# Performance work log

Measured on AMD Instinct MI355X. Metric: run time of the kernel, lower is better.

Reference implementation:

```python
import jax, jax.numpy as jnp
import numpy as np

E = 500_000   # total flattened ngram-node occurrences
N = 100_000   # nr_cfg_nodes
D = 256       # cfg_node_encoding_dim


def setup_inputs() -> dict:
    key = jax.random.key(0)
    ks = jax.random.split(key, 6)
    scattered_input = jax.random.normal(ks[0], (E, D), dtype=jnp.float32)
    previous_cfg_nodes_encodings = jax.random.normal(ks[1], (N, D), dtype=jnp.float32)
    W_k = jax.random.normal(ks[2], (D, D), dtype=jnp.float32) / np.float32(np.sqrt(D))
    b_k = jnp.zeros((D,), dtype=jnp.float32)
    W_g = jax.random.normal(ks[3], (2 * D, D), dtype=jnp.float32) / np.float32(np.sqrt(2 * D))
    b_g = jnp.zeros((D,), dtype=jnp.float32)
    indices = jax.random.randint(ks[4], (E,), 0, N, dtype=jnp.int32)
    return {
        "scattered_input": scattered_input,
        "previous_cfg_nodes_encodings": previous_cfg_nodes_encodings,
        "W_k": W_k, "b_k": b_k, "W_g": W_g, "b_g": b_g,
        "indices": indices,
        "nr_cfg_nodes": N,
    }


def reference(scattered_input, previous_cfg_nodes_encodings, W_k, b_k, W_g, b_g, indices, nr_cfg_nodes):
    d = scattered_input.shape[-1]
    # --- ScatterCombiner, method='attn': scatter-softmax attention per CFG node ---
    keys = scattered_input @ W_k + b_k                       # [E, D]
    queries = previous_cfg_nodes_encodings[indices]          # [E, D] gather per occurrence
    scores = jnp.sum(keys * queries, axis=-1) * (1.0 / jnp.sqrt(jnp.float32(d)))  # [E]
    seg_max = jax.ops.segment_max(scores, indices, num_segments=nr_cfg_nodes)     # [N]
    seg_max = jnp.where(jnp.isfinite(seg_max), seg_max, jnp.float32(0.0))         # empty segments
    ex = jnp.exp(scores - seg_max[indices])                  # [E]
    denom = jax.ops.segment_sum(ex, indices, num_segments=nr_cfg_nodes)           # [N]
    probs = ex / jnp.maximum(denom[indices], jnp.float32(1e-9))                   # [E]
    combined = jax.ops.segment_sum(probs[:, None] * scattered_input, indices,
                                   num_segments=nr_cfg_nodes)                     # [N, D]
    # --- StateUpdater: GRU-like sigmoid gate (dropout disabled / eval mode) ---
    gate_in = jnp.concatenate([previous_cfg_nodes_encodings, combined], axis=-1)  # [N, 2D]
    gate = jax.nn.sigmoid(gate_in @ W_g + b_g)               # [N, D]
    return gate * previous_cfg_nodes_encodings + (1.0 - gate) * combined
```

## Files before the change

### kernel.cpp

```cpp
#include <hip/hip_runtime.h>
#include <math.h>

#define D 256
#define LDS_STRIDE 40

typedef __attribute__((ext_vector_type(8))) short short8;
typedef __attribute__((ext_vector_type(4))) float f32x4;

__device__ inline unsigned short f2bf(float f) {
    unsigned int u = __float_as_uint(f);
    u += 0x7fff + ((u >> 16) & 1);
    return (unsigned short)(u >> 16);
}
__device__ inline float bf2f(unsigned short h) {
    return __uint_as_float(((unsigned int)h) << 16);
}

__global__ __launch_bounds__(256)
void k_prep(const float* __restrict__ prev, const float* __restrict__ Wk,
            const float* __restrict__ Wg,
            unsigned short* __restrict__ prev_bf, unsigned short* __restrict__ Wk_bf,
            unsigned short* __restrict__ WgT, int* __restrict__ counts,
            int n8, int nWk8, int Nn, int gPrev, int gWk, int gWgT) {
    int b = blockIdx.x;
    int t = threadIdx.x;
    if (b < gPrev) {
        int i = b * 256 + t;
        if (i < n8) {
            const float4* p = (const float4*)(prev + (size_t)i * 8);
            float4 a = p[0], c = p[1];
            ushort4 o0 = { f2bf(a.x), f2bf(a.y), f2bf(a.z), f2bf(a.w) };
            ushort4 o1 = { f2bf(c.x), f2bf(c.y), f2bf(c.z), f2bf(c.w) };
            ushort4* q = (ushort4*)(prev_bf + (size_t)i * 8);
            q[0] = o0; q[1] = o1;
        }
    } else if (b < gPrev + gWk) {
        int i = (b - gPrev) * 256 + t;
        if (i < nWk8) {
            const float4* p = (const float4*)(Wk + (size_t)i * 8);
            float4 a = p[0], c = p[1];
            ushort4 o0 = { f2bf(a.x), f2bf(a.y), f2bf(a.z), f2bf(a.w) };
            ushort4 o1 = { f2bf(c.x), f2bf(c.y), f2bf(c.z), f2bf(c.w) };
            ushort4* q = (ushort4*)(Wk_bf + (size_t)i * 8);
            q[0] = o0; q[1] = o1;
        }
    } else if (b < gPrev + gWk + gWgT) {
        int r = b - gPrev - gWk;
        int c = t;
        WgT[(size_t)c * (2 * D) + r] = f2bf(Wg[(size_t)r * D + c]);
    } else {
        int i = (b - gPrev - gWk - gWgT) * 256 + t;
        if (i < Nn) counts[i] = 0;
    }
}

template <int K, bool GATE>
__global__ __launch_bounds__(256)
void k_mfma_gemm(const unsigned short* __restrict__ A0,
                 const unsigned short* __restrict__ A1,
                 const unsigned short* __restrict__ Bn,
                 const float* __restrict__ bg,
                 const float* __restrict__ prevf,
                 unsigned short* __restrict__ wq_out,
                 float* __restrict__ outp,
                 int Nrows) {
    __shared__ unsigned short As[64 * LDS_STRIDE];
    __shared__ unsigned short Bs[256 * LDS_STRIDE];

    int tid  = threadIdx.x;
    int wave = tid >> 6;
    int lane = tid & 63;
    int lcol = lane & 15;
    int quad = lane >> 4;
    int row0 = blockIdx.x * 64;

    f32x4 acc[4][4];
    #pragma unroll
    for (int i = 0; i < 4; i++)
        #pragma unroll
        for (int j = 0; j < 4; j++) acc[i][j] = (f32x4){0.f, 0.f, 0.f, 0.f};

    int arow = tid >> 2, ako = (tid & 3) * 8;
    int grow = row0 + arow;

    for (int kk = 0; kk < K; kk += 32) {
        const unsigned short* Asrc = A0;
        int kc = kk;
        if (GATE && kk >= 256) { Asrc = A1; kc = kk - 256; }

        uint4 av = make_uint4(0u, 0u, 0u, 0u);
        if (grow < Nrows) av = *(const uint4*)&Asrc[(size_t)grow * D + kc + ako];
        *(uint4*)&As[arow * LDS_STRIDE + ako] = av;

        #pragma unroll
        for (int i = 0; i < 4; i++) {
            int c = tid + i * 256;
            int brow = c >> 2, bko = (c & 3) * 8;
            *(uint4*)&Bs[brow * LDS_STRIDE + bko] =
                *(const uint4*)&Bn[(size_t)brow * K + kk + bko];
        }
        __syncthreads();

        short8 a[4], b[4];
        #pragma unroll
        for (int mf = 0; mf < 4; mf++)
            a[mf] = *(const short8*)&As[(mf * 16 + lcol) * LDS_STRIDE + quad * 8];
        #pragma unroll
        for (int nf = 0; nf < 4; nf++)
            b[nf] = *(const short8*)&Bs[(wave * 64 + nf * 16 + lcol) * LDS_STRIDE + quad * 8];
        #pragma unroll
        for (int mf = 0; mf < 4; mf++)
            #pragma unroll
            for (int nf = 0; nf < 4; nf++)
                acc[mf][nf] = __builtin_amdgcn_mfma_f32_16x16x32_bf16(
                    a[mf], b[nf], acc[mf][nf], 0, 0, 0);
        __syncthreads();
    }

    if (!GATE) {
        #pragma unroll
        for (int mf = 0; mf < 4; mf++) {
            #pragma unroll
            for (int nf = 0; nf < 4; nf++) {
                int col = wave * 64 + nf * 16 + lcol;
                #pragma unroll
                for (int r = 0; r < 4; r++) {
                    int gr = row0 + mf * 16 + quad * 4 + r;
                    if (gr < Nrows)
                        wq_out[(size_t)gr * D + col] = f2bf(acc[mf][nf][r]);
                }
            }
        }
    } else {
        float bgv[4];
        #pragma unroll
        for (int nf = 0; nf < 4; nf++) bgv[nf] = bg[wave * 64 + nf * 16 + lcol];
        #pragma unroll
        for (int mf = 0; mf < 4; mf++) {
            #pragma unroll
            for (int nf = 0; nf < 4; nf++) {
                int col = wave * 64 + nf * 16 + lcol;
                #pragma unroll
                for (int r = 0; r < 4; r++) {
                    int gr = row0 + mf * 16 + quad * 4 + r;
                    if (gr < Nrows) {
                        size_t o = (size_t)gr * D + col;
                        float logit = acc[mf][nf][r] + bgv[nf];
                        float g = 1.f / (1.f + __expf(-logit));
                        float cb = bf2f(A1[o]);
                        outp[o] = g * prevf[o] + (1.f - g) * cb;
                    }
                }
            }
        }
    }
}

__global__ __launch_bounds__(256)
void k_hist(const int* __restrict__ idx, int* __restrict__ counts,
            int* __restrict__ rank, int E_) {
    int e = blockIdx.x * 256 + threadIdx.x;
    if (e < E_) rank[e] = atomicAdd(&counts[idx[e]], 1);
}

__global__ __launch_bounds__(256)
void k_part(const int* __restrict__ counts, int* __restrict__ chunkSums, int Nn) {
    __shared__ int sd[256];
    int base = blockIdx.x * 1024;
    int t = threadIdx.x;
    int s = 0;
    #pragma unroll
    for (int i = 0; i < 4; i++) {
        int g = base + t + i * 256;
        if (g < Nn) s += counts[g];
    }
    sd[t] = s;
    __syncthreads();
    for (int st = 128; st; st >>= 1) {
        if (t < st) sd[t] += sd[t + st];
        __syncthreads();
    }
    if (t == 0) chunkSums[blockIdx.x] = sd[0];
}

__global__ __launch_bounds__(256)
void k_top(const int* __restrict__ cs, int* __restrict__ co, int P,
           int* __restrict__ offsets, int Nn, int E_) {
    __shared__ int carry;
    __shared__ int ws[4];
    int t = threadIdx.x, lane = t & 63, w = t >> 6;
    if (t == 0) carry = 0;
    __syncthreads();
    for (int base = 0; base < P; base += 256) {
        int i = base + t;
        int v = (i < P) ? cs[i] : 0;
        int orig = v;
        for (int off = 1; off < 64; off <<= 1) {
            int u = __shfl_up(v, off, 64);
            if (lane >= off) v += u;
        }
        if (lane == 63) ws[w] = v;
        __syncthreads();
        int wex = 0;
        for (int k = 0; k < w; k++) wex += ws[k];
        int incl = v + wex;
        if (i < P) co[i] = carry + incl - orig;
        __syncthreads();
        if (t == 255) carry += incl;
        __syncthreads();
    }
    if (t == 0) offsets[Nn] = E_;
}

__global__ __launch_bounds__(256)
void k_off(const int* __restrict__ counts, const int* __restrict__ chunkOff,
           int* __restrict__ offsets, int Nn) {
    int t = threadIdx.x, lane = t & 63, w = t >> 6;
    int base = blockIdx.x * 1024 + t * 4;
    int c[4]; int ts = 0;
    #pragma unroll
    for (int j = 0; j < 4; j++) {
        int g = base + j;
        c[j] = (g < Nn) ? counts[g] : 0;
        ts += c[j];
    }
    int v = ts;
    for (int off = 1; off < 64; off <<= 1) {
        int u = __shfl_up(v, off, 64);
        if (lane >= off) v += u;
    }
    __shared__ int ws[4];
    if (lane == 63) ws[w] = v;
    __syncthreads();
    int wex = 0;
    for (int k = 0; k < w; k++) wex += ws[k];
    int run = chunkOff[blockIdx.x] + wex + v - ts;
    #pragma unroll
    for (int j = 0; j < 4; j++) {
        int g = base + j;
        if (g < Nn) offsets[g] = run;
        run += c[j];
    }
}

__global__ __launch_bounds__(256)
void k_scatter(const int* __restrict__ idx, const int* __restrict__ rank,
               const int* __restrict__ offsets, int* __restrict__ perm, int E_) {
    int e = blockIdx.x * 256 + threadIdx.x;
    if (e < E_) perm[offsets[idx[e]] + rank[e]] = e;
}

__global__ __launch_bounds__(256)
void k_combine(const float* __restrict__ scat, const unsigned short* __restrict__ wq,
               const int* __restrict__ offsets, const int* __restrict__ perm,
               unsigned short* __restrict__ comb, int Nnodes) {
    int wave = threadIdx.x >> 6;
    int lane = threadIdx.x & 63;
    int n = blockIdx.x * 4 + wave;
    if (n >= Nnodes) return;

    ushort4 wu = *(const ushort4*)&wq[(size_t)n * D + lane * 4];
    float4 wqv = { bf2f(wu.x), bf2f(wu.y), bf2f(wu.z), bf2f(wu.w) };
    int beg = offsets[n], end = offsets[n + 1];

    float m = -INFINITY, l = 0.f;
    float4 acc = { 0.f, 0.f, 0.f, 0.f };
    const float scale = 0.0625f;

    if (beg < end) {
        int e0 = perm[beg];
        float4 sv0 = *(const float4*)&scat[(size_t)e0 * D + lane * 4];
        float4 sv1 = sv0;
        if (beg + 1 < end) {
            int e1 = perm[beg + 1];
            sv1 = *(const float4*)&scat[(size_t)e1 * D + lane * 4];
        }
        for (int pos = beg; pos < end; ++pos) {
            float4 cur = sv0;
            sv0 = sv1;
            if (pos + 2 < end) {
                int e2 = perm[pos + 2];
                sv1 = *(const float4*)&scat[(size_t)e2 * D + lane * 4];
            }
            float d = fmaf(cur.x, wqv.x, fmaf(cur.y, wqv.y,
                      fmaf(cur.z, wqv.z, cur.w * wqv.w)));
            #pragma unroll
            for (int off = 32; off; off >>= 1) d += __shfl_xor(d, off, 64);
            float score = d * scale;
            float nm = fmaxf(m, score);
            float al = __expf(m - nm);
            float p  = __expf(score - nm);
            l = fmaf(l, al, p);
            acc.x = fmaf(acc.x, al, p * cur.x);
            acc.y = fmaf(acc.y, al, p * cur.y);
            acc.z = fmaf(acc.z, al, p * cur.z);
            acc.w = fmaf(acc.w, al, p * cur.w);
            m = nm;
        }
    }
    float inv = 1.f / fmaxf(l, 1e-9f);
    ushort4 o = { f2bf(acc.x * inv), f2bf(acc.y * inv),
                  f2bf(acc.z * inv), f2bf(acc.w * inv) };
    *(ushort4*)&comb[(size_t)n * D + lane * 4] = o;
}

extern "C" void kernel_launch(void* const* d_in, const int* in_sizes, int n_in,
                              void* d_out, int out_size, void* d_ws, size_t ws_size,
                              hipStream_t stream) {
    const float* scat = (const float*)d_in[0];
    const float* prev = (const float*)d_in[1];
    const float* Wk   = (const float*)d_in[2];
    const float* Wg   = (const float*)d_in[4];
    const float* bg   = (const float*)d_in[5];
    const int*   idx  = (const int*)d_in[6];

    const int E_ = in_sizes[6];
    const int Nn = in_sizes[1] / D;

    float* out = (float*)d_out;

    char* w = (char*)d_ws;
    auto alloc = [&](size_t bytes) -> char* {
        char* p = w;
        w += (bytes + 255) & ~(size_t)255;
        return p;
    };
    unsigned short* prev_bf = (unsigned short*)alloc((size_t)Nn * D * 2);
    unsigned short* wq_bf   = (unsigned short*)alloc((size_t)Nn * D * 2);
    unsigned short* comb_bf = (unsigned short*)alloc((size_t)Nn * D * 2);
    unsigned short* Wk_bf   = (unsigned short*)alloc((size_t)D * D * 2);
    unsigned short* WgT_bf  = (unsigned short*)alloc((size_t)2 * D * D * 2);
    int*   counts    = (int*)alloc((size_t)Nn * 4);
    int*   offsets   = (int*)alloc(((size_t)Nn + 1) * 4);
    int    P         = (Nn + 1023) / 1024;
    int*   chunkSums = (int*)alloc((size_t)P * 4);
    int*   chunkOff  = (int*)alloc((size_t)P * 4);
    int*   rank      = (int*)alloc((size_t)E_ * 4);
    int*   perm      = (int*)alloc((size_t)E_ * 4);

    int n8    = Nn * D / 8;
    int nWk8  = D * D / 8;
    int gPrev = (n8 + 255) / 256;
    int gWk   = (nWk8 + 255) / 256;
    int gWgT  = 2 * D;
    int gCnt  = (Nn + 255) / 256;
    k_prep<<<gPrev + gWk + gWgT + gCnt, 256, 0, stream>>>(
        prev, Wk, Wg, prev_bf, Wk_bf, WgT_bf, counts,
        n8, nWk8, Nn, gPrev, gWk, gWgT);

    int gb = (E_ + 255) / 256;
    k_hist<<<gb, 256, 0, stream>>>(idx, counts, rank, E_);
    k_part<<<P, 256, 0, stream>>>(counts, chunkSums, Nn);
    k_top<<<1, 256, 0, stream>>>(chunkSums, chunkOff, P, offsets, Nn, E_);
    k_off<<<P, 256, 0, stream>>>(counts, chunkOff, offsets, Nn);
    k_scatter<<<gb, 256, 0, stream>>>(idx, rank, offsets, perm, E_);

    int gm = (Nn + 63) / 64;
    k_mfma_gemm<256, false><<<gm, 256, 0, stream>>>(
        prev_bf, nullptr, Wk_bf, nullptr, nullptr, wq_bf, nullptr, Nn);

    k_combine<<<(Nn + 3) / 4, 256, 0, stream>>>(scat, wq_bf, offsets, perm, comb_bf, Nn);

    k_mfma_gemm<512, true><<<gm, 256, 0, stream>>>(
        prev_bf, comb_bf, WgT_bf, bg, prev, nullptr, out, Nn);
}
```

Baseline: 998.5 us.

## Fuse bf16 conversion into GEMM loads, merge scan kernels, co-launch scatter with GEMM

The separate pass that converted prev to bf16 is removed. The GEMMs now read fp32 prev and convert it while loading tiles into LDS. The three-kernel prefix scan becomes one kernel in which each block re-sums all earlier counts itself. The permutation scatter and the Wk GEMM share one launch as disjoint block ranges, and the combine loop prefetches one row deeper. Together these cut launches and a full N×D round trip, in exchange for redundant prefix reads and twice the A-tile load bytes.

Measured after the change: 1.007 ms. No clear change (+0.8%).

```diff
diff --git a/kernel.cpp b/kernel.cpp
--- a/kernel.cpp
+++ b/kernel.cpp
@@ -17,25 +17,13 @@
 }
 
 __global__ __launch_bounds__(256)
-void k_prep(const float* __restrict__ prev, const float* __restrict__ Wk,
-            const float* __restrict__ Wg,
-            unsigned short* __restrict__ prev_bf, unsigned short* __restrict__ Wk_bf,
-            unsigned short* __restrict__ WgT, int* __restrict__ counts,
-            int n8, int nWk8, int Nn, int gPrev, int gWk, int gWgT) {
+void k_prep(const float* __restrict__ Wk, const float* __restrict__ Wg,
+            unsigned short* __restrict__ Wk_bf, unsigned short* __restrict__ WgT,
+            int* __restrict__ counts, int nWk8, int Nn, int gWk, int gWgT) {
     int b = blockIdx.x;
     int t = threadIdx.x;
-    if (b < gPrev) {
+    if (b < gWk) {
         int i = b * 256 + t;
-        if (i < n8) {
-            const float4* p = (const float4*)(prev + (size_t)i * 8);
-            float4 a = p[0], c = p[1];
-            ushort4 o0 = { f2bf(a.x), f2bf(a.y), f2bf(a.z), f2bf(a.w) };
-            ushort4 o1 = { f2bf(c.x), f2bf(c.y), f2bf(c.z), f2bf(c.w) };
-            ushort4* q = (ushort4*)(prev_bf + (size_t)i * 8);
-            q[0] = o0; q[1] = o1;
-        }
-    } else if (b < gPrev + gWk) {
-        int i = (b - gPrev) * 256 + t;
         if (i < nWk8) {
             const float4* p = (const float4*)(Wk + (size_t)i * 8);
             float4 a = p[0], c = p[1];
@@ -44,26 +32,26 @@
             ushort4* q = (ushort4*)(Wk_bf + (size_t)i * 8);
             q[0] = o0; q[1] = o1;
         }
-    } else if (b < gPrev + gWk + gWgT) {
-        int r = b - gPrev - gWk;
+    } else if (b < gWk + gWgT) {
+        int r = b - gWk;
         int c = t;
         WgT[(size_t)c * (2 * D) + r] = f2bf(Wg[(size_t)r * D + c]);
     } else {
-        int i = (b - gPrev - gWk - gWgT) * 256 + t;
+        int i = (b - gWk - gWgT) * 256 + t;
         if (i < Nn) counts[i] = 0;
     }
 }
 
 template <int K, bool GATE>
-__global__ __launch_bounds__(256)
-void k_mfma_gemm(const unsigned short* __restrict__ A0,
-                 const unsigned short* __restrict__ A1,
-                 const unsigned short* __restrict__ Bn,
-                 const float* __restrict__ bg,
-                 const float* __restrict__ prevf,
-                 unsigned short* __restrict__ wq_out,
-                 float* __restrict__ outp,
-                 int Nrows) {
+__device__ __forceinline__ void gemm_body(
+        const float* __restrict__ Af,
+        const unsigned short* __restrict__ A1,
+        const unsigned short* __restrict__ Bn,
+        const float* __restrict__ bg,
+        const float* __restrict__ prevf,
+        unsigned short* __restrict__ wq_out,
+        float* __restrict__ outp,
+        int Nrows, int blk) {
     __shared__ unsigned short As[64 * LDS_STRIDE];
     __shared__ unsigned short Bs[256 * LDS_STRIDE];
 
@@ -72,7 +60,7 @@
     int lane = tid & 63;
     int lcol = lane & 15;
     int quad = lane >> 4;
-    int row0 = blockIdx.x * 64;
+    int row0 = blk * 64;
 
     f32x4 acc[4][4];
     #pragma unroll
@@ -84,13 +72,21 @@
     int grow = row0 + arow;
 
     for (int kk = 0; kk < K; kk += 32) {
-        const unsigned short* Asrc = A0;
-        int kc = kk;
-        if (GATE && kk >= 256) { Asrc = A1; kc = kk - 256; }
-
-        uint4 av = make_uint4(0u, 0u, 0u, 0u);
-        if (grow < Nrows) av = *(const uint4*)&Asrc[(size_t)grow * D + kc + ako];
-        *(uint4*)&As[arow * LDS_STRIDE + ako] = av;
+        ushort4 h0 = {0, 0, 0, 0}, h1 = {0, 0, 0, 0};
+        if (grow < Nrows) {
+            if (!GATE || kk < 256) {
+                const float* s = &Af[(size_t)grow * D + kk + ako];
+                float4 f0 = *(const float4*)s;
+                float4 f1 = *(const float4*)(s + 4);
+                h0 = (ushort4){ f2bf(f0.x), f2bf(f0.y), f2bf(f0.z), f2bf(f0.w) };
+                h1 = (ushort4){ f2bf(f1.x), f2bf(f1.y), f2bf(f1.z), f2bf(f1.w) };
+            } else {
+                const ushort4* s = (const ushort4*)&A1[(size_t)grow * D + (kk - 256) + ako];
+                h0 = s[0]; h1 = s[1];
+            }
+        }
+        *(ushort4*)&As[arow * LDS_STRIDE + ako]     = h0;
+        *(ushort4*)&As[arow * LDS_STRIDE + ako + 4] = h1;
 
         #pragma unroll
         for (int i = 0; i < 4; i++) {
@@ -157,6 +153,13 @@
 }
 
 __global__ __launch_bounds__(256)
+void k_gemm_gate(const float* __restrict__ prev, const unsigned short* __restrict__ comb,
+                 const unsigned short* __restrict__ WgT, const float* __restrict__ bg,
+                 float* __restrict__ outp, int Nrows) {
+    gemm_body<512, true>(prev, comb, WgT, bg, prev, nullptr, outp, Nrows, blockIdx.x);
+}
+
+__global__ __launch_bounds__(256)
 void k_hist(const int* __restrict__ idx, int* __restrict__ counts,
             int* __restrict__ rank, int E_) {
     int e = blockIdx.x * 256 + threadIdx.x;
@@ -164,63 +167,28 @@
 }
 
 __global__ __launch_bounds__(256)
-void k_part(const int* __restrict__ counts, int* __restrict__ chunkSums, int Nn) {
+void k_scan(const int* __restrict__ counts, int* __restrict__ offsets,
+            int Nn, int E_) {
     __shared__ int sd[256];
-    int base = blockIdx.x * 1024;
-    int t = threadIdx.x;
+    __shared__ int ws[4];
+    int b = blockIdx.x, t = threadIdx.x, lane = t & 63, w = t >> 6;
+
+    int pre = b * 1024;
     int s = 0;
-    #pragma unroll
-    for (int i = 0; i < 4; i++) {
-        int g = base + t + i * 256;
-        if (g < Nn) s += counts[g];
-    }
+    for (int i = t; i < pre; i += 256) s += counts[i];
     sd[t] = s;
     __syncthreads();
     for (int st = 128; st; st >>= 1) {
         if (t < st) sd[t] += sd[t + st];
         __syncthreads();
     }
-    if (t == 0) chunkSums[blockIdx.x] = sd[0];
-}
-
-__global__ __launch_bounds__(256)
-void k_top(const int* __restrict__ cs, int* __restrict__ co, int P,
-           int* __restrict__ offsets, int Nn, int E_) {
-    __shared__ int carry;
-    __shared__ int ws[4];
-    int t = threadIdx.x, lane = t & 63, w = t >> 6;
-    if (t == 0) carry = 0;
-    __syncthreads();
-    for (int base = 0; base < P; base += 256) {
-        int i = base + t;
-        int v = (i < P) ? cs[i] : 0;
-        int orig = v;
-        for (int off = 1; off < 64; off <<= 1) {
-            int u = __shfl_up(v, off, 64);
-            if (lane >= off) v += u;
-        }
-        if (lane == 63) ws[w] = v;
-        __syncthreads();
-        int wex = 0;
-        for (int k = 0; k < w; k++) wex += ws[k];
-        int incl = v + wex;
-        if (i < P) co[i] = carry + incl - orig;
-        __syncthreads();
-        if (t == 255) carry += incl;
-        __syncthreads();
-    }
-    if (t == 0) offsets[Nn] = E_;
-}
-
-__global__ __launch_bounds__(256)
-void k_off(const int* __restrict__ counts, const int* __restrict__ chunkOff,
-           int* __restrict__ offsets, int Nn) {
-    int t = threadIdx.x, lane = t & 63, w = t >> 6;
-    int base = blockIdx.x * 1024 + t * 4;
+    int base = sd[0];
+
+    int g0 = b * 1024 + t * 4;
     int c[4]; int ts = 0;
     #pragma unroll
     for (int j = 0; j < 4; j++) {
-        int g = base + j;
+        int g = g0 + j;
         c[j] = (g < Nn) ? counts[g] : 0;
         ts += c[j];
     }
@@ -229,25 +197,33 @@
         int u = __shfl_up(v, off, 64);
         if (lane >= off) v += u;
     }
-    __shared__ int ws[4];
     if (lane == 63) ws[w] = v;
     __syncthreads();
     int wex = 0;
     for (int k = 0; k < w; k++) wex += ws[k];
-    int run = chunkOff[blockIdx.x] + wex + v - ts;
+    int run = base + wex + v - ts;
     #pragma unroll
     for (int j = 0; j < 4; j++) {
-        int g = base + j;
+        int g = g0 + j;
         if (g < Nn) offsets[g] = run;
         run += c[j];
     }
-}
-
-__global__ __launch_bounds__(256)
-void k_scatter(const int* __restrict__ idx, const int* __restrict__ rank,
-               const int* __restrict__ offsets, int* __restrict__ perm, int E_) {
-    int e = blockIdx.x * 256 + threadIdx.x;
-    if (e < E_) perm[offsets[idx[e]] + rank[e]] = e;
+    if (b == 0 && t == 0) offsets[Nn] = E_;
+}
+
+__global__ __launch_bounds__(256)
+void k_fused1(const int* __restrict__ idx, const int* __restrict__ rank,
+              const int* __restrict__ offsets, int* __restrict__ perm, int E_,
+              const float* __restrict__ prev, const unsigned short* __restrict__ Wk_bf,
+              unsigned short* __restrict__ wq_bf, int Nrows, int gm) {
+    int b = blockIdx.x;
+    if (b < gm) {
+        gemm_body<256, false>(prev, nullptr, Wk_bf, nullptr, nullptr, wq_bf, nullptr,
+                              Nrows, b);
+    } else {
+        int e = (b - gm) * 256 + threadIdx.x;
+        if (e < E_) perm[offsets[idx[e]] + rank[e]] = e;
+    }
 }
 
 __global__ __launch_bounds__(256)
@@ -268,19 +244,17 @@
     const float scale = 0.0625f;
 
     if (beg < end) {
-        int e0 = perm[beg];
-        float4 sv0 = *(const float4*)&scat[(size_t)e0 * D + lane * 4];
-        float4 sv1 = sv0;
-        if (beg + 1 < end) {
-            int e1 = perm[beg + 1];
-            sv1 = *(const float4*)&scat[(size_t)e1 * D + lane * 4];
-        }
+        float4 sv0 = *(const float4*)&scat[(size_t)perm[beg] * D + lane * 4];
+        float4 sv1 = sv0, sv2 = sv0;
+        if (beg + 1 < end) sv1 = *(const float4*)&scat[(size_t)perm[beg + 1] * D + lane * 4];
+        if (beg + 2 < end) sv2 = *(const float4*)&scat[(size_t)perm[beg + 2] * D + lane * 4];
+        int ea = (beg + 3 < end) ? perm[beg + 3] : 0;
         for (int pos = beg; pos < end; ++pos) {
             float4 cur = sv0;
-            sv0 = sv1;
-            if (pos + 2 < end) {
-                int e2 = perm[pos + 2];
-                sv1 = *(const float4*)&scat[(size_t)e2 * D + lane * 4];
+            sv0 = sv1; sv1 = sv2;
+            if (pos + 3 < end) {
+                sv2 = *(const float4*)&scat[(size_t)ea * D + lane * 4];
+                ea = (pos + 4 < end) ? perm[pos + 4] : 0;
             }
             float d = fmaf(cur.x, wqv.x, fmaf(cur.y, wqv.y,
                       fmaf(cur.z, wqv.z, cur.w * wqv.w)));
@@ -325,42 +299,34 @@
         w += (bytes + 255) & ~(size_t)255;
         return p;
     };
-    unsigned short* prev_bf = (unsigned short*)alloc((size_t)Nn * D * 2);
     unsigned short* wq_bf   = (unsigned short*)alloc((size_t)Nn * D * 2);
     unsigned short* comb_bf = (unsigned short*)alloc((size_t)Nn * D * 2);
     unsigned short* Wk_bf   = (unsigned short*)alloc((size_t)D * D * 2);
     unsigned short* WgT_bf  = (unsigned short*)alloc((size_t)2 * D * D * 2);
     int*   counts    = (int*)alloc((size_t)Nn * 4);
     int*   offsets   = (int*)alloc(((size_t)Nn + 1) * 4);
-    int    P         = (Nn + 1023) / 1024;
-    int*   chunkSums = (int*)alloc((size_t)P * 4);
-    int*   chunkOff  = (int*)alloc((size_t)P * 4);
     int*   rank      = (int*)alloc((size_t)E_ * 4);
     int*   perm      = (int*)alloc((size_t)E_ * 4);
 
-    int n8    = Nn * D / 8;
     int nWk8  = D * D / 8;
-    int gPrev = (n8 + 255) / 256;
     int gWk   = (nWk8 + 255) / 256;
     int gWgT  = 2 * D;
     int gCnt  = (Nn + 255) / 256;
-    k_prep<<<gPrev + gWk + gWgT + gCnt, 256, 0, stream>>>(
-        prev, Wk, Wg, prev_bf, Wk_bf, WgT_bf, counts,
-        n8, nWk8, Nn, gPrev, gWk, gWgT);
+    k_prep<<<gWk + gWgT + gCnt, 256, 0, stream>>>(
+        Wk, Wg, Wk_bf, WgT_bf, counts, nWk8, Nn, gWk, gWgT);
 
     int gb = (E_ + 255) / 256;
     k_hist<<<gb, 256, 0, stream>>>(idx, counts, rank, E_);
-    k_part<<<P, 256, 0, stream>>>(counts, chunkSums, Nn);
-    k_top<<<1, 256, 0, stream>>>(chunkSums, chunkOff, P, offsets, Nn, E_);
-    k_off<<<P, 256, 0, stream>>>(counts, chunkOff, offsets, Nn);
-    k_scatter<<<gb, 256, 0, stream>>>(idx, rank, offsets, perm, E_);
-
-    int gm = (Nn + 63) / 64;
-    k_mfma_gemm<256, false><<<gm, 256, 0, stream>>>(
-        prev_bf, nullptr, Wk_bf, nullptr, nullptr, wq_bf, nullptr, Nn);
+
+    int P = (Nn + 1023) / 1024;
+    k_scan<<<P, 256, 0, stream>>>(counts, offsets, Nn, E_);
+
+    int gm  = (Nn + 63) / 64;
+    int gSc = (E_ + 255) / 256;
+    k_fused1<<<gm + gSc, 256, 0, stream>>>(
+        idx, rank, offsets, perm, E_, prev, Wk_bf, wq_bf, Nn, gm);
 
     k_combine<<<(Nn + 3) / 4, 256, 0, stream>>>(scat, wq_bf, offsets, perm, comb_bf, Nn);
 
-    k_mfma_gemm<512, true><<<gm, 256, 0, stream>>>(
-        prev_bf, comb_bf, WgT_bf, bg, prev, nullptr, out, Nn);
-}
+    k_gemm_gate<<<gm, 256, 0, stream>>>(prev, comb_bf, WgT_bf, bg, out, Nn);
+}
```
